# Kernel tuning notes

Measured on AMD Instinct MI355X. Metric: run time of the kernel, lower is better.

The kernel has to match this reference:

```python
import jax, jax.numpy as jnp
import numpy as np

B, N, OBS, H, HEADS = 8192, 32, 128, 256, 4
HD = H // HEADS  # head dim = 64
GAIN = (0.125 / H) ** 0.5
LN_EPS = 1e-5


def _ln(x):
    # LayerNorm over last dim, no affine (elementwise_affine=False)
    m = x.mean(axis=-1, keepdims=True)
    v = ((x - m) ** 2).mean(axis=-1, keepdims=True)
    return (x - m) * jax.lax.rsqrt(v + LN_EPS)


def setup_inputs() -> dict:
    key = jax.random.key(0)
    ks = jax.random.split(key, 20)
    f32 = jnp.float32
    # weights stored (in, out) so y = x @ W + b (transpose of torch layout)
    def w(k, i, o, g):
        return (jax.random.normal(k, (i, o), dtype=f32) * g)
    inp = {
        "all_agent_obs": jax.random.normal(ks[0], (B, N, OBS), dtype=f32),
        # EntityEmbedding (obs-only): 1-layer LinearEncoder, normal init * t-fixup gain
        "W_emb": w(ks[1], OBS, H, GAIN), "b_emb": jnp.zeros((H,), f32),
        # ResidualSelfAttention projections
        "Wq": w(ks[2], H, H, GAIN), "bq": jnp.zeros((H,), f32),
        "Wk": w(ks[3], H, H, GAIN), "bk": jnp.zeros((H,), f32),
        "Wv": w(ks[4], H, H, GAIN), "bv": jnp.zeros((H,), f32),
        "Wo": w(ks[5], H, H, GAIN), "bo": jnp.zeros((H,), f32),
        # LinearEncoder tail (num_layers=2), kaiming-ish scale * t-fixup gain
        "W1": w(ks[6], H, H, GAIN), "b1": jnp.zeros((H,), f32),
        "W2": w(ks[7], H, H, GAIN), "b2": jnp.zeros((H,), f32),
        # value head: Linear(h_size + 1, 1)
        "Wval": w(ks[8], H + 1, 1, (1.0 / (H + 1)) ** 0.5), "bval": jnp.zeros((1,), f32),
    }
    return inp


def reference(all_agent_obs, W_emb, b_emb, Wq, bq, Wk, bk, Wv, bv, Wo, bo,
              W1, b1, W2, b2, Wval, bval):
    # --- EntityEmbedding: 1-layer MLP with SiLU ---
    ent = jax.nn.silu(jnp.einsum("bno,oh->bnh", all_agent_obs, W_emb) + b_emb)

    # --- ResidualSelfAttention (pre-norm, no mask) ---
    x = _ln(ent)                                        # embedding_norm
    q = (x @ Wq + bq).reshape(B, N, HEADS, HD)
    k = (x @ Wk + bk).reshape(B, N, HEADS, HD)
    v = (x @ Wv + bv).reshape(B, N, HEADS, HD)
    attn = jnp.einsum("bnhd,bmhd->bhnm", q, k) / jnp.sqrt(jnp.float32(HD))
    attn = jax.nn.softmax(attn, axis=-1)
    out = jnp.einsum("bhnm,bmhd->bnhd", attn, v).reshape(B, N, H)
    out = _ln(out @ Wo + bo + x)                        # fc_out + residual, residual_norm
    pooled = out.mean(axis=1)                           # (B, H) unmasked avg pool

    # --- LinearEncoder tail (2 layers, SiLU) ---
    enc = jax.nn.silu(pooled @ W1 + b1)
    enc = jax.nn.silu(enc @ W2 + b2)

    # --- norm agent count: max_agents updates to N, so val = N*2/N - 1 = 1.0 ---
    nc = jnp.ones((B, 1), dtype=enc.dtype)
    enc = jnp.concatenate([enc, nc], axis=-1)           # (B, H+1)
    return enc @ Wval + bval                            # (B, 1)
```

## Files before the change

### kernel.cpp

```cpp
#include <hip/hip_runtime.h>


typedef __bf16 bf16x8 __attribute__((ext_vector_type(8)));
typedef float f32x4 __attribute__((ext_vector_type(4)));
typedef unsigned short ushort_t;

#define DEVI static __device__ __forceinline__
#define MFMA16(a, b, cc) __builtin_amdgcn_mfma_f32_16x16x32_bf16((a), (b), (cc), 0, 0, 0)

#define WAITV2 asm volatile("s_waitcnt vmcnt(2)" ::: "memory")
#define WAITV0 asm volatile("s_waitcnt vmcnt(0)" ::: "memory")
#define WAITLG asm volatile("s_waitcnt lgkmcnt(0)" ::: "memory")
#define BAR() __builtin_amdgcn_s_barrier()
#define SCHEDB() __builtin_amdgcn_sched_barrier(0)

constexpr int OWemb_ = 0;
constexpr int OWq_   = 32768;
constexpr int OWk_   = OWq_ + 65536;
constexpr int OWv_   = OWk_ + 65536;
constexpr int OWo_   = OWv_ + 65536;
constexpr int OW1_   = OWo_ + 65536;
constexpr int OW2_   = OW1_ + 65536;

constexpr int OBS_STRIDE = 264;
constexpr int L_BST = 32768;
constexpr int LDS_TOTAL = 32768 + 3 * 16384;
static_assert(LDS_TOTAL <= 81920, "need <=80KB for 2 blocks/CU");

DEVI float silu_f(float x) { return x / (1.0f + __expf(-x)); }
DEVI f32x4 splat4(float x) { f32x4 v = {x, x, x, x}; return v; }
DEVI uint2 pack4(f32x4 v) {
  union { __bf16 h[4]; uint2 u; } x;
  x.h[0] = (__bf16)v[0]; x.h[1] = (__bf16)v[1];
  x.h[2] = (__bf16)v[2]; x.h[3] = (__bf16)v[3];
  return x.u;
}
DEVI f32x4 unpk(uint2 u) {
  union { uint2 u2; __bf16 h[4]; } x; x.u2 = u;
  f32x4 v = {(float)x.h[0], (float)x.h[1], (float)x.h[2], (float)x.h[3]};
  return v;
}
DEVI bf16x8 ld_frag(const char* p) { return *(const bf16x8*)p; }
DEVI bf16x8 u4b(unsigned a, unsigned b, unsigned cc, unsigned d) {
  union { unsigned u[4]; bf16x8 v; } x;
  x.u[0] = a; x.u[1] = b; x.u[2] = cc; x.u[3] = d;
  return x.v;
}
DEVI unsigned to_agpr(unsigned v) {
  unsigned d;
  asm volatile("v_accvgpr_write_b32 %0, %1" : "=a"(d) : "v"(v));
  return d;
}
DEVI unsigned from_agpr(unsigned a) {
  unsigned d;
  asm volatile("v_accvgpr_read_b32 %0, %1" : "=v"(d) : "a"(a));
  return d;
}
DEVI int xaddr(int row, int k4) {
  int t = row >> 4, cc = row & 15;
  int ks = k4 >> 5, kg = (k4 >> 3) & 3, half = (k4 >> 2) & 1;
  return ((t * 8 + ks) * 64 + kg * 16 + cc) * 16 + half * 8;
}

typedef const __attribute__((address_space(1))) unsigned int* gas_ptr;
typedef __attribute__((address_space(3))) unsigned int* las_ptr;
DEVI void gload16(const void* g, void* l) {
  __builtin_amdgcn_global_load_lds((gas_ptr)g, (las_ptr)l, 16, 0, 0);
}

constexpr int CSRC(int p) {
  return (p < 4)  ? (OWemb_ + p * 8192)
       : (p < 12) ? (OWq_ + (p - 4) * 8192)
       : (p < 20) ? (OWk_ + (p - 12) * 8192)
       : (p < 28) ? (OWv_ + (p - 20) * 8192)
                  : (OWo_ + (p - 28) * 8192);
}

DEVI void issue_chunk(const ushort_t* pw, int srcOff, char* bst, int slot, int wv, int lane) {
  char* dst = bst + slot * 16384 + wv * 2048;
  const ushort_t* s = pw + srcOff + wv * 1024 + (size_t)lane * 8;
  gload16(s, dst);
  gload16(s + 512, dst + 1024);
}
#define PH_ISSUE(ch) issue_chunk(pw, CSRC(ch), bst, (ch) % 3, wv, lane)

__global__ void pack_weights(const float* __restrict__ Wemb, const float* __restrict__ Wq,
                             const float* __restrict__ Wk, const float* __restrict__ Wv,
                             const float* __restrict__ Wo, const float* __restrict__ W1,
                             const float* __restrict__ W2, ushort_t* __restrict__ ws) {
  int t = blockIdx.x * 256 + threadIdx.x;
  if (t >= 53248) return;
  const float* src;
  int dst, n, k0;
  if (t < 4096) {
    int rem = t & 1023;
    int ctg = rem >> 6, l = rem & 63;
    n = ctg * 16 + (l & 15);
    k0 = (t >> 10) * 32 + (l >> 4) * 8;
    src = Wemb; dst = OWemb_ + t * 8;
  } else if (t < 36864) {
    int u = t - 4096, m = u >> 13, loc = u & 8191;
    int rem = loc & 1023;
    int ctg = rem >> 6, l = rem & 63;
    n = ctg * 16 + (l & 15);
    k0 = (loc >> 10) * 32 + (l >> 4) * 8;
    src = (m == 0) ? Wq : (m == 1) ? Wk : (m == 2) ? Wv : Wo;
    dst = OWq_ + m * 65536 + loc * 8;
  } else {
    int u = t - 36864, m = u >> 13, loc = u & 8191;
    int ln = loc & 63, ks = (loc >> 6) & 7, ct = loc >> 9;
    n = ct * 16 + (ln & 15);
    k0 = ks * 32 + (ln >> 4) * 8;
    src = m ? W2 : W1; dst = OW1_ + m * 65536 + loc * 8;
  }
  union { __bf16 h[8]; uint4 u; } pk;
  #pragma unroll
  for (int j = 0; j < 8; ++j) pk.h[j] = (__bf16)src[(k0 + j) * 256 + n];
  *(uint4*)(ws + dst) = pk.u;
}

__global__ __launch_bounds__(512, 4)
void poca_fused(const float* __restrict__ obs, const ushort_t* __restrict__ pw,
                const float* __restrict__ b_emb, const float* __restrict__ bq,
                const float* __restrict__ bk, const float* __restrict__ bv,
                const float* __restrict__ bo, const float* __restrict__ b1,
                const float* __restrict__ b2, const float* __restrict__ Wval,
                const float* __restrict__ bval, float* __restrict__ out) {
  __shared__ __align__(128) char lds[LDS_TOTAL];
  const int tid = threadIdx.x;
  const int wv = tid >> 6, lane = tid & 63;
  const int g = lane >> 4, c = lane & 15;
  const int mg = wv >> 2, ng = wv & 3;
  char* xb = lds;
  char* bst = lds + L_BST;
  char* as_ = bst + wv * 4096;
  char* pp1 = bst;
  char* poolb = bst;
  char* y1b = bst + 8448;
  char* ptlb = bst + 16896;
  char* pp2 = bst + 20480;

  PH_ISSUE(0); PH_ISSUE(1);
  f32x4 bemb_r[4];
  #pragma unroll
  for (int ct = 0; ct < 4; ++ct) bemb_r[ct] = *(const f32x4*)(b_emb + ng * 64 + ct * 16 + g * 4);

  {
    const float4* op = (const float4*)(obs + (size_t)blockIdx.x * 64 * 128);
    #pragma unroll
    for (int it = 0; it < 4; ++it) {
      int idx = it * 512 + tid;
      float4 v = op[idx];
      int row = idx >> 5, col4 = idx & 31;
      union { __bf16 h[4]; uint2 u; } cv;
      cv.h[0] = (__bf16)v.x; cv.h[1] = (__bf16)v.y;
      cv.h[2] = (__bf16)v.z; cv.h[3] = (__bf16)v.w;
      *(uint2*)(xb + row * OBS_STRIDE + col4 * 8) = cv.u;
    }
  }
  WAITLG;

  f32x4 acc[2][4];

  #pragma unroll
  for (int p = 0; p < 4; ++p) {
    WAITV2; BAR();
    PH_ISSUE(p + 2);
    if (p == 0) {
      #pragma unroll
      for (int ct = 0; ct < 4; ++ct) { acc[0][ct] = bemb_r[ct]; acc[1][ct] = bemb_r[ct]; }
    }
    const char* ck = bst + (p % 3) * 16384;
    bf16x8 wf[4], xf[2];
    #pragma unroll
    for (int t = 0; t < 4; ++t) wf[t] = ld_frag(ck + ((ng * 4 + t) * 64 + lane) * 16);
    #pragma unroll
    for (int rt = 0; rt < 2; ++rt)
      xf[rt] = ld_frag(xb + ((mg * 2 + rt) * 16 + c) * OBS_STRIDE + p * 64 + g * 16);
    #pragma unroll
    for (int rt = 0; rt < 2; ++rt)
      #pragma unroll
      for (int ct = 0; ct < 4; ++ct) acc[rt][ct] = MFMA16(wf[ct], xf[rt], acc[rt][ct]);
    SCHEDB();
  }

  BAR();
  #pragma unroll
  for (int rt = 0; rt < 2; ++rt)
    #pragma unroll
    for (int ct = 0; ct < 4; ++ct)
      #pragma unroll
      for (int r = 0; r < 4; ++r) acc[rt][ct][r] = silu_f(acc[rt][ct][r]);
  #pragma unroll
  for (int rt = 0; rt < 2; ++rt) {
    float s1 = 0.f, s2 = 0.f;
    #pragma unroll
    for (int ct = 0; ct < 4; ++ct)
      #pragma unroll
      for (int r = 0; r < 4; ++r) { float e = acc[rt][ct][r]; s1 += e; s2 += e * e; }
    s1 += __shfl_xor(s1, 16); s2 += __shfl_xor(s2, 16);
    s1 += __shfl_xor(s1, 32); s2 += __shfl_xor(s2, 32);
    if (g == 0)
      *(float2*)(pp1 + (mg * 32 + rt * 16 + c) * 32 + ng * 8) = make_float2(s1, s2);
  }
  WAITLG; BAR();
  {
    float mu[2], rs[2];
    #pragma unroll
    for (int rt = 0; rt < 2; ++rt) {
      int row = mg * 32 + rt * 16 + c;
      f32x4 pA = *(const f32x4*)(pp1 + row * 32);
      f32x4 pB = *(const f32x4*)(pp1 + row * 32 + 16);
      float S1 = pA[0] + pA[2] + pB[0] + pB[2];
      float S2 = pA[1] + pA[3] + pB[1] + pB[3];
      float m_ = S1 * (1.f / 256.f);
      float v_ = S2 * (1.f / 256.f) - m_ * m_;
      mu[rt] = m_; rs[rt] = rsqrtf(v_ + 1e-5f);
    }
    #pragma unroll
    for (int rt = 0; rt < 2; ++rt)
      #pragma unroll
      for (int ct = 0; ct < 4; ++ct) {
        f32x4 xv;
        #pragma unroll
        for (int r = 0; r < 4; ++r) xv[r] = (acc[rt][ct][r] - mu[rt]) * rs[rt];
        *(uint2*)(xb + xaddr(mg * 32 + rt * 16 + c, ng * 64 + ct * 16 + g * 4)) = pack4(xv);
      }
  }
  f32x4 bq_r[4];
  #pragma unroll
  for (int ct = 0; ct < 4; ++ct) bq_r[ct] = *(const f32x4*)(bq + ng * 64 + ct * 16 + g * 4);
  SCHEDB();
  WAITLG; BAR();

  #pragma unroll
  for (int p = 4; p < 12; ++p) {
    WAITV2; BAR();
    PH_ISSUE(p + 2);
    if (p == 4) {
      #pragma unroll
      for (int ct = 0; ct < 4; ++ct) { acc[0][ct] = bq_r[ct]; acc[1][ct] = bq_r[ct]; }
    }
    const char* ck = bst + (p % 3) * 16384;
    const int ks = p - 4;
    bf16x8 wf[4], xf[2];
    #pragma unroll
    for (int t = 0; t < 4; ++t) wf[t] = ld_frag(ck + ((ng * 4 + t) * 64 + lane) * 16);
    #pragma unroll
    for (int rt = 0; rt < 2; ++rt)
      xf[rt] = ld_frag(xb + (((mg * 2 + rt) * 8 + ks) * 64 + lane) * 16);
    #pragma unroll
    for (int rt = 0; rt < 2; ++rt)
      #pragma unroll
      for (int ct = 0; ct < 4; ++ct) acc[rt][ct] = MFMA16(wf[ct], xf[rt], acc[rt][ct]);
    SCHEDB();
  }

  unsigned qs[16];
  #pragma unroll
  for (int rt = 0; rt < 2; ++rt)
    #pragma unroll
    for (int ct = 0; ct < 4; ++ct) {
      uint2 qp = pack4(acc[rt][ct]);
      qs[(rt * 4 + ct) * 2] = to_agpr(qp.x);
      qs[(rt * 4 + ct) * 2 + 1] = to_agpr(qp.y);
    }
  f32x4 bk_r[4];
  #pragma unroll
  for (int ct = 0; ct < 4; ++ct) bk_r[ct] = *(const f32x4*)(bk + ng * 64 + ct * 16 + g * 4);

  #pragma unroll
  for (int p = 12; p < 20; ++p) {
    if (p < 19) { WAITV2; } else { WAITV0; }
    BAR();
    if (p <= 17) PH_ISSUE(p + 2);
    if (p == 12) {
      #pragma unroll
      for (int ct = 0; ct < 4; ++ct) { acc[0][ct] = bk_r[ct]; acc[1][ct] = bk_r[ct]; }
    }
    const char* ck = bst + (p % 3) * 16384;
    const int ks = p - 12;
    bf16x8 wf[4], xf[2];
    #pragma unroll
    for (int t = 0; t < 4; ++t) wf[t] = ld_frag(ck + ((ng * 4 + t) * 64 + lane) * 16);
    #pragma unroll
    for (int rt = 0; rt < 2; ++rt)
      xf[rt] = ld_frag(xb + (((mg * 2 + rt) * 8 + ks) * 64 + lane) * 16);
    #pragma unroll
    for (int rt = 0; rt < 2; ++rt)
      #pragma unroll
      for (int ct = 0; ct < 4; ++ct) acc[rt][ct] = MFMA16(wf[ct], xf[rt], acc[rt][ct]);
    SCHEDB();
  }

  uint2 p_pk[2][2];
  float bv_r[4];
  {
    BAR();
    PH_ISSUE(20);
    f32x4 sacc[2][2];
    sacc[0][0] = splat4(0.f); sacc[0][1] = splat4(0.f);
    sacc[1][0] = splat4(0.f); sacc[1][1] = splat4(0.f);
    #pragma unroll
    for (int hf = 0; hf < 2; ++hf) {
      #pragma unroll
      for (int rt2 = 0; rt2 < 2; ++rt2)
        #pragma unroll
        for (int ctl = 0; ctl < 2; ++ctl) {
          int gr = ctl * 2 + (g >> 1);
          int off = rt2 * 1024 + (gr * 16 + c) * 16 + (g & 1) * 8;
          int qi = (rt2 * 4 + hf * 2 + ctl) * 2;
          *(uint2*)(as_ + off) = make_uint2(from_agpr(qs[qi]), from_agpr(qs[qi + 1]));
          *(uint2*)(as_ + 2048 + off) = pack4(acc[rt2][hf * 2 + ctl]);
        }
      WAITLG;
      bf16x8 qf[2], kf[2];
      #pragma unroll
      for (int t = 0; t < 2; ++t) {
        qf[t] = ld_frag(as_ + t * 1024 + lane * 16);
        kf[t] = ld_frag(as_ + 2048 + t * 1024 + lane * 16);
      }
      #pragma unroll
      for (int qt = 0; qt < 2; ++qt)
        #pragma unroll
        for (int kt = 0; kt < 2; ++kt)
          sacc[qt][kt] = MFMA16(kf[kt], qf[qt], sacc[qt][kt]);
    }
    #pragma unroll
    for (int qt = 0; qt < 2; ++qt) {
      float sc[2][4];
      float mx = -3e38f;
      #pragma unroll
      for (int kt = 0; kt < 2; ++kt)
        #pragma unroll
        for (int r = 0; r < 4; ++r) { sc[kt][r] = sacc[qt][kt][r] * 0.125f; mx = fmaxf(mx, sc[kt][r]); }
      mx = fmaxf(mx, __shfl_xor(mx, 16));
      mx = fmaxf(mx, __shfl_xor(mx, 32));
      float sm = 0.f;
      #pragma unroll
      for (int kt = 0; kt < 2; ++kt)
        #pragma unroll
        for (int r = 0; r < 4; ++r) { float e = __expf(sc[kt][r] - mx); sc[kt][r] = e; sm += e; }
      sm += __shfl_xor(sm, 16);
      sm += __shfl_xor(sm, 32);
      float ri = 1.0f / sm;
      #pragma unroll
      for (int kt = 0; kt < 2; ++kt) {
        f32x4 pv = {sc[kt][0] * ri, sc[kt][1] * ri, sc[kt][2] * ri, sc[kt][3] * ri};
        p_pk[qt][kt] = pack4(pv);
      }
    }
    #pragma unroll
    for (int ct = 0; ct < 4; ++ct) bv_r[ct] = bv[ng * 64 + ct * 16 + c];
  }
  SCHEDB();
  WAITLG; BAR();
  PH_ISSUE(21);

  #pragma unroll
  for (int p = 20; p < 28; ++p) {
    if (p < 27) { WAITV2; } else { WAITV0; }
    BAR();
    if (p <= 25) PH_ISSUE(p + 2);
    if (p == 20) {
      #pragma unroll
      for (int ct = 0; ct < 4; ++ct) {
        f32x4 b_ = splat4(bv_r[ct]);
        acc[0][ct] = b_; acc[1][ct] = b_;
      }
    }
    const char* ck = bst + (p % 3) * 16384;
    const int ks = p - 20;
    bf16x8 wf[4], xf[2];
    #pragma unroll
    for (int t = 0; t < 4; ++t) wf[t] = ld_frag(ck + ((ng * 4 + t) * 64 + lane) * 16);
    #pragma unroll
    for (int rt = 0; rt < 2; ++rt)
      xf[rt] = ld_frag(xb + (((mg * 2 + rt) * 8 + ks) * 64 + lane) * 16);
    #pragma unroll
    for (int rt = 0; rt < 2; ++rt)
      #pragma unroll
      for (int ct = 0; ct < 4; ++ct) acc[rt][ct] = MFMA16(xf[rt], wf[ct], acc[rt][ct]);
    SCHEDB();
  }

  {
    BAR();
    #pragma unroll
    for (int rt2 = 0; rt2 < 2; ++rt2)
      #pragma unroll
      for (int ct = 0; ct < 4; ++ct) {
        int gr = rt2 * 2 + (g >> 1);
        int off = ct * 1024 + (gr * 16 + c) * 16 + (g & 1) * 8;
        *(uint2*)(as_ + off) = pack4(acc[rt2][ct]);
      }
    uint2 respk[2][4];
    #pragma unroll
    for (int rt = 0; rt < 2; ++rt)
      #pragma unroll
      for (int ct = 0; ct < 4; ++ct)
        respk[rt][ct] = *(uint2*)(xb + xaddr(mg * 32 + rt * 16 + c, ng * 64 + ct * 16 + g * 4));
    WAITLG;
    bf16x8 vf[4];
    #pragma unroll
    for (int dt = 0; dt < 4; ++dt) vf[dt] = ld_frag(as_ + dt * 1024 + lane * 16);
    const int l1 = (g & 1) * 32 + c, l2 = l1 + 16;
    const bool hi = (g >= 2);
    #pragma unroll
    for (int qt = 0; qt < 2; ++qt) {
      unsigned x0k0 = __shfl(p_pk[qt][0].x, l1), x0k1 = __shfl(p_pk[qt][1].x, l1);
      unsigned y0k0 = __shfl(p_pk[qt][0].y, l1), y0k1 = __shfl(p_pk[qt][1].y, l1);
      unsigned x1k0 = __shfl(p_pk[qt][0].x, l2), x1k1 = __shfl(p_pk[qt][1].x, l2);
      unsigned y1k0 = __shfl(p_pk[qt][0].y, l2), y1k1 = __shfl(p_pk[qt][1].y, l2);
      bf16x8 pf = u4b(hi ? x0k1 : x0k0, hi ? y0k1 : y0k0, hi ? x1k1 : x1k0, hi ? y1k1 : y1k0);
      #pragma unroll
      for (int dt = 0; dt < 4; ++dt) {
        f32x4 o = splat4(0.f);
        o = MFMA16(vf[dt], pf, o);
        *(uint2*)(xb + xaddr(mg * 32 + qt * 16 + c, ng * 64 + dt * 16 + g * 4)) = pack4(o);
      }
    }
    f32x4 bo_r[4];
    #pragma unroll
    for (int ct = 0; ct < 4; ++ct) bo_r[ct] = *(const f32x4*)(bo + ng * 64 + ct * 16 + g * 4);
    #pragma unroll
    for (int ct = 0; ct < 4; ++ct) {
      #pragma unroll
      for (int rt = 0; rt < 2; ++rt) acc[rt][ct] = bo_r[ct] + unpk(respk[rt][ct]);
    }
  }
  SCHEDB();
  WAITLG; BAR();
  PH_ISSUE(28); PH_ISSUE(29);

  #pragma unroll
  for (int p = 28; p < 36; ++p) {
    if (p < 35) { WAITV2; } else { WAITV0; }
    BAR();
    if (p <= 33) PH_ISSUE(p + 2);
    const char* ck = bst + (p % 3) * 16384;
    const int ks = p - 28;
    bf16x8 wf[4], xf[2];
    #pragma unroll
    for (int t = 0; t < 4; ++t) wf[t] = ld_frag(ck + ((ng * 4 + t) * 64 + lane) * 16);
    #pragma unroll
    for (int rt = 0; rt < 2; ++rt)
      xf[rt] = ld_frag(xb + (((mg * 2 + rt) * 8 + ks) * 64 + lane) * 16);
    #pragma unroll
    for (int rt = 0; rt < 2; ++rt)
      #pragma unroll
      for (int ct = 0; ct < 4; ++ct) acc[rt][ct] = MFMA16(wf[ct], xf[rt], acc[rt][ct]);
    SCHEDB();
  }

  BAR();
  #pragma unroll
  for (int rt = 0; rt < 2; ++rt) {
    float s1 = 0.f, s2 = 0.f;
    #pragma unroll
    for (int ct = 0; ct < 4; ++ct)
      #pragma unroll
      for (int r = 0; r < 4; ++r) { float e = acc[rt][ct][r]; s1 += e; s2 += e * e; }
    s1 += __shfl_xor(s1, 16); s2 += __shfl_xor(s2, 16);
    s1 += __shfl_xor(s1, 32); s2 += __shfl_xor(s2, 32);
    if (g == 0)
      *(float2*)(pp2 + (mg * 32 + rt * 16 + c) * 32 + ng * 8) = make_float2(s1, s2);
  }
  WAITLG; BAR();
  {
    float mu[2], rs[2];
    #pragma unroll
    for (int rt = 0; rt < 2; ++rt) {
      int row = mg * 32 + rt * 16 + c;
      f32x4 pA = *(const f32x4*)(pp2 + row * 32);
      f32x4 pB = *(const f32x4*)(pp2 + row * 32 + 16);
      float S1 = pA[0] + pA[2] + pB[0] + pB[2];
      float S2 = pA[1] + pA[3] + pB[1] + pB[3];
      float m_ = S1 * (1.f / 256.f);
      float v_ = S2 * (1.f / 256.f) - m_ * m_;
      mu[rt] = m_; rs[rt] = rsqrtf(v_ + 1e-5f);
    }
    f32x4 ps[4];
    #pragma unroll
    for (int ct = 0; ct < 4; ++ct) {
      #pragma unroll
      for (int r = 0; r < 4; ++r)
        ps[ct][r] = (acc[0][ct][r] - mu[0]) * rs[0] + (acc[1][ct][r] - mu[1]) * rs[1];
    }
    #pragma unroll
    for (int st = 1; st < 16; st <<= 1)
      #pragma unroll
      for (int ct = 0; ct < 4; ++ct)
        #pragma unroll
        for (int r = 0; r < 4; ++r) ps[ct][r] += __shfl_xor(ps[ct][r], st);
    if (c == 0) {
      #pragma unroll
      for (int ct = 0; ct < 4; ++ct) {
        f32x4 pv;
        #pragma unroll
        for (int r = 0; r < 4; ++r) pv[r] = ps[ct][r] * (1.f / 32.f);
        *(uint2*)(poolb + mg * 528 + (ng * 64 + ct * 16 + g * 4) * 2) = pack4(pv);
      }
    }
  }
  #pragma unroll
  for (int it = 0; it < 4; ++it) {
    int idx = it * 512 + tid;
    if (idx < 1792) {
      int row = 2 + (idx >> 7), col = idx & 127;
      *(unsigned*)(poolb + row * 528 + col * 4) = 0;
      *(unsigned*)(y1b + row * 528 + col * 4) = 0;
    }
  }
  WAITLG; BAR();

  f32x4 t1[2];
  #pragma unroll
  for (int ctl = 0; ctl < 2; ++ctl) t1[ctl] = splat4(b1[wv * 32 + ctl * 16 + c]);
  #pragma unroll
  for (int ks = 0; ks < 8; ++ks) {
    bf16x8 a = ld_frag(poolb + c * 528 + ks * 64 + g * 16);
    #pragma unroll
    for (int ctl = 0; ctl < 2; ++ctl) {
      bf16x8 b = *(const bf16x8*)(pw + OW1_ + (size_t)(((wv * 2 + ctl) * 8 + ks) * 64 + lane) * 8);
      t1[ctl] = MFMA16(a, b, t1[ctl]);
    }
  }
  if (g == 0) {
    #pragma unroll
    for (int ctl = 0; ctl < 2; ++ctl)
      #pragma unroll
      for (int r = 0; r < 4; ++r)
        *(__bf16*)(y1b + r * 528 + (wv * 32 + ctl * 16 + c) * 2) = (__bf16)silu_f(t1[ctl][r]);
  }
  WAITLG; BAR();
  f32x4 t2[2];
  #pragma unroll
  for (int ctl = 0; ctl < 2; ++ctl) t2[ctl] = splat4(b2[wv * 32 + ctl * 16 + c]);
  #pragma unroll
  for (int ks = 0; ks < 8; ++ks) {
    bf16x8 a = ld_frag(y1b + c * 528 + ks * 64 + g * 16);
    #pragma unroll
    for (int ctl = 0; ctl < 2; ++ctl) {
      bf16x8 b = *(const bf16x8*)(pw + OW2_ + (size_t)(((wv * 2 + ctl) * 8 + ks) * 64 + lane) * 8);
      t2[ctl] = MFMA16(a, b, t2[ctl]);
    }
  }
  if (g == 0) {
    float part[4] = {0.f, 0.f, 0.f, 0.f};
    #pragma unroll
    for (int ctl = 0; ctl < 2; ++ctl) {
      float wvv = Wval[wv * 32 + ctl * 16 + c];
      #pragma unroll
      for (int r = 0; r < 4; ++r) part[r] += silu_f(t2[ctl][r]) * wvv;
    }
    #pragma unroll
    for (int m = 1; m < 16; m <<= 1) {
      #pragma unroll
      for (int r = 0; r < 4; ++r) part[r] += __shfl_xor(part[r], m);
    }
    if (c == 0) {
      float4 p4 = make_float4(part[0], part[1], part[2], part[3]);
      *(float4*)(ptlb + wv * 16) = p4;
    }
  }
  WAITLG; BAR();
  if (tid < 2) {
    float s = Wval[256] + bval[0];
    const float* pt = (const float*)ptlb;
    #pragma unroll
    for (int w8 = 0; w8 < 8; ++w8) s += pt[w8 * 4 + tid];
    out[(size_t)blockIdx.x * 2 + tid] = s;
  }
}

extern "C" void kernel_launch(void* const* d_in, const int* in_sizes, int n_in,
                              void* d_out, int out_size, void* d_ws, size_t ws_size,
                              hipStream_t stream) {
  (void)in_sizes; (void)n_in; (void)out_size; (void)ws_size;
  const float* obs  = (const float*)d_in[0];
  const float* Wemb = (const float*)d_in[1];
  const float* bemb = (const float*)d_in[2];
  const float* Wq   = (const float*)d_in[3];
  const float* bq   = (const float*)d_in[4];
  const float* Wk   = (const float*)d_in[5];
  const float* bk   = (const float*)d_in[6];
  const float* Wv   = (const float*)d_in[7];
  const float* bv   = (const float*)d_in[8];
  const float* Wo   = (const float*)d_in[9];
  const float* bo   = (const float*)d_in[10];
  const float* W1   = (const float*)d_in[11];
  const float* b1   = (const float*)d_in[12];
  const float* W2   = (const float*)d_in[13];
  const float* b2   = (const float*)d_in[14];
  const float* Wval = (const float*)d_in[15];
  const float* bval = (const float*)d_in[16];
  ushort_t* ws = (ushort_t*)d_ws;
  float* out = (float*)d_out;

  pack_weights<<<208, 256, 0, stream>>>(Wemb, Wq, Wk, Wv, Wo, W1, W2, ws);
  poca_fused<<<4096, 512, 0, stream>>>(obs, ws, bemb, bq, bk, bv, bo, b1, b2, Wval, bval, out);
}
```

Baseline: 312.3 us.

## Load weight fragments directly from global memory instead of LDS triple-buffering

Removes the global_load_lds triple-buffered staging of weight chunks and their per-chunk barriers and waits. Each wave now reads its MFMA weight fragments straight from global (L2-cached) memory inside the GEMM loops. LDS use drops to 66KB and the partial-sum buffer moves to a dedicated region. This cuts barrier and LDS traffic overhead, but it exposes global load latency inside the MFMA loops with no explicit prefetch. The weights are also no longer shared across the block's waves through LDS.

```diff
diff --git a/kernel.cpp b/kernel.cpp
--- a/kernel.cpp
+++ b/kernel.cpp
@@ -8,8 +8,6 @@
 #define DEVI static __device__ __forceinline__
 #define MFMA16(a, b, cc) __builtin_amdgcn_mfma_f32_16x16x32_bf16((a), (b), (cc), 0, 0, 0)
 
-#define WAITV2 asm volatile("s_waitcnt vmcnt(2)" ::: "memory")
-#define WAITV0 asm volatile("s_waitcnt vmcnt(0)" ::: "memory")
 #define WAITLG asm volatile("s_waitcnt lgkmcnt(0)" ::: "memory")
 #define BAR() __builtin_amdgcn_s_barrier()
 #define SCHEDB() __builtin_amdgcn_sched_barrier(0)
@@ -23,8 +21,9 @@
 constexpr int OW2_   = OW1_ + 65536;
 
 constexpr int OBS_STRIDE = 264;
-constexpr int L_BST = 32768;
-constexpr int LDS_TOTAL = 32768 + 3 * 16384;
+constexpr int L_SCR = 32768;
+constexpr int L_PP  = 65536;
+constexpr int LDS_TOTAL = 65536 + 2048;
 static_assert(LDS_TOTAL <= 81920, "need <=80KB for 2 blocks/CU");
 
 DEVI float silu_f(float x) { return x / (1.0f + __expf(-x)); }
@@ -41,6 +40,7 @@
   return v;
 }
 DEVI bf16x8 ld_frag(const char* p) { return *(const bf16x8*)p; }
+DEVI bf16x8 ld_fragg(const ushort_t* p) { return *(const bf16x8*)p; }
 DEVI bf16x8 u4b(unsigned a, unsigned b, unsigned cc, unsigned d) {
   union { unsigned u[4]; bf16x8 v; } x;
   x.u[0] = a; x.u[1] = b; x.u[2] = cc; x.u[3] = d;
@@ -61,28 +61,6 @@
   int ks = k4 >> 5, kg = (k4 >> 3) & 3, half = (k4 >> 2) & 1;
   return ((t * 8 + ks) * 64 + kg * 16 + cc) * 16 + half * 8;
 }
-
-typedef const __attribute__((address_space(1))) unsigned int* gas_ptr;
-typedef __attribute__((address_space(3))) unsigned int* las_ptr;
-DEVI void gload16(const void* g, void* l) {
-  __builtin_amdgcn_global_load_lds((gas_ptr)g, (las_ptr)l, 16, 0, 0);
-}
-
-constexpr int CSRC(int p) {
-  return (p < 4)  ? (OWemb_ + p * 8192)
-       : (p < 12) ? (OWq_ + (p - 4) * 8192)
-       : (p < 20) ? (OWk_ + (p - 12) * 8192)
-       : (p < 28) ? (OWv_ + (p - 20) * 8192)
-                  : (OWo_ + (p - 28) * 8192);
-}
-
-DEVI void issue_chunk(const ushort_t* pw, int srcOff, char* bst, int slot, int wv, int lane) {
-  char* dst = bst + slot * 16384 + wv * 2048;
-  const ushort_t* s = pw + srcOff + wv * 1024 + (size_t)lane * 8;
-  gload16(s, dst);
-  gload16(s + 512, dst + 1024);
-}
-#define PH_ISSUE(ch) issue_chunk(pw, CSRC(ch), bst, (ch) % 3, wv, lane)
 
 __global__ void pack_weights(const float* __restrict__ Wemb, const float* __restrict__ Wq,
                              const float* __restrict__ Wk, const float* __restrict__ Wv,
@@ -132,15 +110,15 @@
   const int g = lane >> 4, c = lane & 15;
   const int mg = wv >> 2, ng = wv & 3;
   char* xb = lds;
-  char* bst = lds + L_BST;
-  char* as_ = bst + wv * 4096;
-  char* pp1 = bst;
-  char* poolb = bst;
-  char* y1b = bst + 8448;
-  char* ptlb = bst + 16896;
-  char* pp2 = bst + 20480;
-
-  PH_ISSUE(0); PH_ISSUE(1);
+  char* scr = lds + L_SCR;
+  char* as_ = scr + wv * 4096;
+  char* ppb = lds + L_PP;
+  char* poolb = scr;
+  char* y1b = scr + 8448;
+  char* ptlb = scr + 16896;
+
+  const size_t wqoff = (size_t)((ng * 4) * 64 + lane) * 8;
+
   f32x4 bemb_r[4];
   #pragma unroll
   for (int ct = 0; ct < 4; ++ct) bemb_r[ct] = *(const f32x4*)(b_emb + ng * 64 + ct * 16 + g * 4);
@@ -158,33 +136,30 @@
       *(uint2*)(xb + row * OBS_STRIDE + col4 * 8) = cv.u;
     }
   }
-  WAITLG;
+  WAITLG; BAR();
 
   f32x4 acc[2][4];
 
-  #pragma unroll
-  for (int p = 0; p < 4; ++p) {
-    WAITV2; BAR();
-    PH_ISSUE(p + 2);
-    if (p == 0) {
-      #pragma unroll
-      for (int ct = 0; ct < 4; ++ct) { acc[0][ct] = bemb_r[ct]; acc[1][ct] = bemb_r[ct]; }
-    }
-    const char* ck = bst + (p % 3) * 16384;
-    bf16x8 wf[4], xf[2];
-    #pragma unroll
-    for (int t = 0; t < 4; ++t) wf[t] = ld_frag(ck + ((ng * 4 + t) * 64 + lane) * 16);
-    #pragma unroll
-    for (int rt = 0; rt < 2; ++rt)
-      xf[rt] = ld_frag(xb + ((mg * 2 + rt) * 16 + c) * OBS_STRIDE + p * 64 + g * 16);
-    #pragma unroll
-    for (int rt = 0; rt < 2; ++rt)
-      #pragma unroll
-      for (int ct = 0; ct < 4; ++ct) acc[rt][ct] = MFMA16(wf[ct], xf[rt], acc[rt][ct]);
-    SCHEDB();
-  }
-
-  BAR();
+  {
+    const ushort_t* wsec = pw + OWemb_ + wqoff;
+    #pragma unroll
+    for (int ct = 0; ct < 4; ++ct) { acc[0][ct] = bemb_r[ct]; acc[1][ct] = bemb_r[ct]; }
+    #pragma unroll
+    for (int p = 0; p < 4; ++p) {
+      bf16x8 wf[4], xf[2];
+      #pragma unroll
+      for (int t = 0; t < 4; ++t) wf[t] = ld_fragg(wsec + p * 8192 + t * 512);
+      #pragma unroll
+      for (int rt = 0; rt < 2; ++rt)
+        xf[rt] = ld_frag(xb + ((mg * 2 + rt) * 16 + c) * OBS_STRIDE + p * 64 + g * 16);
+      #pragma unroll
+      for (int rt = 0; rt < 2; ++rt)
+        #pragma unroll
+        for (int ct = 0; ct < 4; ++ct) acc[rt][ct] = MFMA16(wf[ct], xf[rt], acc[rt][ct]);
+    }
+  }
+  SCHEDB();
+
   #pragma unroll
   for (int rt = 0; rt < 2; ++rt)
     #pragma unroll
@@ -201,7 +176,7 @@
     s1 += __shfl_xor(s1, 16); s2 += __shfl_xor(s2, 16);
     s1 += __shfl_xor(s1, 32); s2 += __shfl_xor(s2, 32);
     if (g == 0)
-      *(float2*)(pp1 + (mg * 32 + rt * 16 + c) * 32 + ng * 8) = make_float2(s1, s2);
+      *(float2*)(ppb + (mg * 32 + rt * 16 + c) * 32 + ng * 8) = make_float2(s1, s2);
   }
   WAITLG; BAR();
   {
@@ -209,8 +184,8 @@
     #pragma unroll
     for (int rt = 0; rt < 2; ++rt) {
       int row = mg * 32 + rt * 16 + c;
-      f32x4 pA = *(const f32x4*)(pp1 + row * 32);
-      f32x4 pB = *(const f32x4*)(pp1 + row * 32 + 16);
+      f32x4 pA = *(const f32x4*)(ppb + row * 32);
+      f32x4 pB = *(const f32x4*)(ppb + row * 32 + 16);
       float S1 = pA[0] + pA[2] + pB[0] + pB[2];
       float S2 = pA[1] + pA[3] + pB[1] + pB[3];
       float m_ = S1 * (1.f / 256.f);
@@ -230,30 +205,25 @@
   f32x4 bq_r[4];
   #pragma unroll
   for (int ct = 0; ct < 4; ++ct) bq_r[ct] = *(const f32x4*)(bq + ng * 64 + ct * 16 + g * 4);
-  SCHEDB();
-  WAITLG; BAR();
-
-  #pragma unroll
-  for (int p = 4; p < 12; ++p) {
-    WAITV2; BAR();
-    PH_ISSUE(p + 2);
-    if (p == 4) {
-      #pragma unroll
-      for (int ct = 0; ct < 4; ++ct) { acc[0][ct] = bq_r[ct]; acc[1][ct] = bq_r[ct]; }
-    }
-    const char* ck = bst + (p % 3) * 16384;
-    const int ks = p - 4;
-    bf16x8 wf[4], xf[2];
-    #pragma unroll
-    for (int t = 0; t < 4; ++t) wf[t] = ld_frag(ck + ((ng * 4 + t) * 64 + lane) * 16);
-    #pragma unroll
-    for (int rt = 0; rt < 2; ++rt)
-      xf[rt] = ld_frag(xb + (((mg * 2 + rt) * 8 + ks) * 64 + lane) * 16);
-    #pragma unroll
-    for (int rt = 0; rt < 2; ++rt)
-      #pragma unroll
-      for (int ct = 0; ct < 4; ++ct) acc[rt][ct] = MFMA16(wf[ct], xf[rt], acc[rt][ct]);
-    SCHEDB();
+  WAITLG; BAR();
+
+  {
+    const ushort_t* wsec = pw + OWq_ + wqoff;
+    #pragma unroll
+    for (int ct = 0; ct < 4; ++ct) { acc[0][ct] = bq_r[ct]; acc[1][ct] = bq_r[ct]; }
+    #pragma unroll
+    for (int ks = 0; ks < 8; ++ks) {
+      bf16x8 wf[4], xf[2];
+      #pragma unroll
+      for (int t = 0; t < 4; ++t) wf[t] = ld_fragg(wsec + ks * 8192 + t * 512);
+      #pragma unroll
+      for (int rt = 0; rt < 2; ++rt)
+        xf[rt] = ld_frag(xb + (((mg * 2 + rt) * 8 + ks) * 64 + lane) * 16);
+      #pragma unroll
+      for (int rt = 0; rt < 2; ++rt)
+        #pragma unroll
+        for (int ct = 0; ct < 4; ++ct) acc[rt][ct] = MFMA16(wf[ct], xf[rt], acc[rt][ct]);
+    }
   }
 
   unsigned qs[16];
@@ -269,35 +239,28 @@
   #pragma unroll
   for (int ct = 0; ct < 4; ++ct) bk_r[ct] = *(const f32x4*)(bk + ng * 64 + ct * 16 + g * 4);
 
-  #pragma unroll
-  for (int p = 12; p < 20; ++p) {
-    if (p < 19) { WAITV2; } else { WAITV0; }
-    BAR();
-    if (p <= 17) PH_ISSUE(p + 2);
-    if (p == 12) {
-      #pragma unroll
-      for (int ct = 0; ct < 4; ++ct) { acc[0][ct] = bk_r[ct]; acc[1][ct] = bk_r[ct]; }
-    }
-    const char* ck = bst + (p % 3) * 16384;
-    const int ks = p - 12;
-    bf16x8 wf[4], xf[2];
-    #pragma unroll
-    for (int t = 0; t < 4; ++t) wf[t] = ld_frag(ck + ((ng * 4 + t) * 64 + lane) * 16);
-    #pragma unroll
-    for (int rt = 0; rt < 2; ++rt)
-      xf[rt] = ld_frag(xb + (((mg * 2 + rt) * 8 + ks) * 64 + lane) * 16);
-    #pragma unroll
-    for (int rt = 0; rt < 2; ++rt)
-      #pragma unroll
-      for (int ct = 0; ct < 4; ++ct) acc[rt][ct] = MFMA16(wf[ct], xf[rt], acc[rt][ct]);
-    SCHEDB();
+  {
+    const ushort_t* wsec = pw + OWk_ + wqoff;
+    #pragma unroll
+    for (int ct = 0; ct < 4; ++ct) { acc[0][ct] = bk_r[ct]; acc[1][ct] = bk_r[ct]; }
+    #pragma unroll
+    for (int ks = 0; ks < 8; ++ks) {
+      bf16x8 wf[4], xf[2];
+      #pragma unroll
+      for (int t = 0; t < 4; ++t) wf[t] = ld_fragg(wsec + ks * 8192 + t * 512);
+      #pragma unroll
+      for (int rt = 0; rt < 2; ++rt)
+        xf[rt] = ld_frag(xb + (((mg * 2 + rt) * 8 + ks) * 64 + lane) * 16);
+      #pragma unroll
+      for (int rt = 0; rt < 2; ++rt)
+        #pragma unroll
+        for (int ct = 0; ct < 4; ++ct) acc[rt][ct] = MFMA16(wf[ct], xf[rt], acc[rt][ct]);
+    }
   }
 
   uint2 p_pk[2][2];
   float bv_r[4];
   {
-    BAR();
-    PH_ISSUE(20);
     f32x4 sacc[2][2];
     sacc[0][0] = splat4(0.f); sacc[0][1] = splat4(0.f);
     sacc[1][0] = splat4(0.f); sacc[1][1] = splat4(0.f);
@@ -353,39 +316,32 @@
     #pragma unroll
     for (int ct = 0; ct < 4; ++ct) bv_r[ct] = bv[ng * 64 + ct * 16 + c];
   }
+
+  {
+    const ushort_t* wsec = pw + OWv_ + wqoff;
+    #pragma unroll
+    for (int ct = 0; ct < 4; ++ct) {
+      f32x4 b_ = splat4(bv_r[ct]);
+      acc[0][ct] = b_; acc[1][ct] = b_;
+    }
+    #pragma unroll
+    for (int ks = 0; ks < 8; ++ks) {
+      bf16x8 wf[4], xf[2];
+      #pragma unroll
+      for (int t = 0; t < 4; ++t) wf[t] = ld_fragg(wsec + ks * 8192 + t * 512);
+      #pragma unroll
+      for (int rt = 0; rt < 2; ++rt)
+        xf[rt] = ld_frag(xb + (((mg * 2 + rt) * 8 + ks) * 64 + lane) * 16);
+      #pragma unroll
+      for (int rt = 0; rt < 2; ++rt)
+        #pragma unroll
+        for (int ct = 0; ct < 4; ++ct) acc[rt][ct] = MFMA16(xf[rt], wf[ct], acc[rt][ct]);
+    }
+  }
   SCHEDB();
-  WAITLG; BAR();
-  PH_ISSUE(21);
-
-  #pragma unroll
-  for (int p = 20; p < 28; ++p) {
-    if (p < 27) { WAITV2; } else { WAITV0; }
-    BAR();
-    if (p <= 25) PH_ISSUE(p + 2);
-    if (p == 20) {
-      #pragma unroll
-      for (int ct = 0; ct < 4; ++ct) {
-        f32x4 b_ = splat4(bv_r[ct]);
-        acc[0][ct] = b_; acc[1][ct] = b_;
-      }
-    }
-    const char* ck = bst + (p % 3) * 16384;
-    const int ks = p - 20;
-    bf16x8 wf[4], xf[2];
-    #pragma unroll
-    for (int t = 0; t < 4; ++t) wf[t] = ld_frag(ck + ((ng * 4 + t) * 64 + lane) * 16);
-    #pragma unroll
-    for (int rt = 0; rt < 2; ++rt)
-      xf[rt] = ld_frag(xb + (((mg * 2 + rt) * 8 + ks) * 64 + lane) * 16);
-    #pragma unroll
-    for (int rt = 0; rt < 2; ++rt)
-      #pragma unroll
-      for (int ct = 0; ct < 4; ++ct) acc[rt][ct] = MFMA16(xf[rt], wf[ct], acc[rt][ct]);
-    SCHEDB();
-  }
-
-  {
-    BAR();
+  BAR();
+
+  {
     #pragma unroll
     for (int rt2 = 0; rt2 < 2; ++rt2)
       #pragma unroll
@@ -429,31 +385,25 @@
       for (int rt = 0; rt < 2; ++rt) acc[rt][ct] = bo_r[ct] + unpk(respk[rt][ct]);
     }
   }
-  SCHEDB();
-  WAITLG; BAR();
-  PH_ISSUE(28); PH_ISSUE(29);
-
-  #pragma unroll
-  for (int p = 28; p < 36; ++p) {
-    if (p < 35) { WAITV2; } else { WAITV0; }
-    BAR();
-    if (p <= 33) PH_ISSUE(p + 2);
-    const char* ck = bst + (p % 3) * 16384;
-    const int ks = p - 28;
-    bf16x8 wf[4], xf[2];
-    #pragma unroll
-    for (int t = 0; t < 4; ++t) wf[t] = ld_frag(ck + ((ng * 4 + t) * 64 + lane) * 16);
-    #pragma unroll
-    for (int rt = 0; rt < 2; ++rt)
-      xf[rt] = ld_frag(xb + (((mg * 2 + rt) * 8 + ks) * 64 + lane) * 16);
-    #pragma unroll
-    for (int rt = 0; rt < 2; ++rt)
-      #pragma unroll
-      for (int ct = 0; ct < 4; ++ct) acc[rt][ct] = MFMA16(wf[ct], xf[rt], acc[rt][ct]);
-    SCHEDB();
-  }
-
-  BAR();
+  WAITLG; BAR();
+
+  {
+    const ushort_t* wsec = pw + OWo_ + wqoff;
+    #pragma unroll
+    for (int ks = 0; ks < 8; ++ks) {
+      bf16x8 wf[4], xf[2];
+      #pragma unroll
+      for (int t = 0; t < 4; ++t) wf[t] = ld_fragg(wsec + ks * 8192 + t * 512);
+      #pragma unroll
+      for (int rt = 0; rt < 2; ++rt)
+        xf[rt] = ld_frag(xb + (((mg * 2 + rt) * 8 + ks) * 64 + lane) * 16);
+      #pragma unroll
+      for (int rt = 0; rt < 2; ++rt)
+        #pragma unroll
+        for (int ct = 0; ct < 4; ++ct) acc[rt][ct] = MFMA16(wf[ct], xf[rt], acc[rt][ct]);
+    }
+  }
+
   #pragma unroll
   for (int rt = 0; rt < 2; ++rt) {
     float s1 = 0.f, s2 = 0.f;
@@ -464,7 +414,7 @@
     s1 += __shfl_xor(s1, 16); s2 += __shfl_xor(s2, 16);
     s1 += __shfl_xor(s1, 32); s2 += __shfl_xor(s2, 32);
     if (g == 0)
-      *(float2*)(pp2 + (mg * 32 + rt * 16 + c) * 32 + ng * 8) = make_float2(s1, s2);
+      *(float2*)(ppb + (mg * 32 + rt * 16 + c) * 32 + ng * 8) = make_float2(s1, s2);
   }
   WAITLG; BAR();
   {
@@ -472,8 +422,8 @@
     #pragma unroll
     for (int rt = 0; rt < 2; ++rt) {
       int row = mg * 32 + rt * 16 + c;
-      f32x4 pA = *(const f32x4*)(pp2 + row * 32);
-      f32x4 pB = *(const f32x4*)(pp2 + row * 32 + 16);
+      f32x4 pA = *(const f32x4*)(ppb + row * 32);
+      f32x4 pB = *(const f32x4*)(ppb + row * 32 + 16);
       float S1 = pA[0] + pA[2] + pB[0] + pB[2];
       float S2 = pA[1] + pA[3] + pB[1] + pB[3];
       float m_ = S1 * (1.f / 256.f);
```

Result: faster. 295.3 us (-5.4%).
